# Kernel tuning notes

Hardware: AMD Instinct MI355X
Metric: run time of the kernel (lower is better)

The kernel has to match this reference:

```python
import jax, jax.numpy as jnp
import numpy as np

N = 50000      # nodes
E = 800000     # edges (avg degree 16)
F_IN = 256
F_OUT = 256


def setup_inputs() -> dict:
    key = jax.random.key(0)
    ks = jax.random.split(key, 8)
    feature = jax.random.normal(ks[0], (N, F_IN), dtype=jnp.float32)
    e_w = jax.random.uniform(ks[1], (E, 1), dtype=jnp.float32)
    snorm_n = jnp.ones((N, 1), dtype=jnp.float32)
    snorm_e = jnp.ones((E, 1), dtype=jnp.float32)
    src = jax.random.randint(ks[2], (E,), 0, N, dtype=jnp.int32)
    dst = jax.random.randint(ks[3], (E,), 0, N, dtype=jnp.int32)
    scale = 1.0 / np.sqrt(F_IN)
    W_self = jax.random.normal(ks[4], (F_IN, F_OUT), dtype=jnp.float32) * scale
    W = jax.random.normal(ks[5], (F_IN, F_OUT), dtype=jnp.float32) * scale
    b = jax.random.normal(ks[6], (F_OUT,), dtype=jnp.float32) * scale
    return {"feature": feature, "e_w": e_w, "snorm_n": snorm_n,
            "snorm_e": snorm_e, "W_self": W_self, "W": W, "b": b,
            "src": src, "dst": dst}


def reference(feature, e_w, snorm_n, snorm_e, W_self, W, b, src, dst):
    n = feature.shape[0]
    ones_e = jnp.ones_like(src, dtype=feature.dtype)
    # self transform
    h_s = feature @ W_self                                   # [N, F_OUT]
    # source-side degree normalization: deg_out^{-1/2}
    out_deg = jnp.maximum(jax.ops.segment_sum(ones_e, src, num_segments=n), 1.0)
    feat = feature * (out_deg ** -0.5)[:, None]              # [N, F_IN]
    # message = h[src] * e_w, aggregated by sum into dst (u_mul_e + sum reduce)
    msgs = feat[src] * e_w                                   # [E, F_IN]
    agg = jax.ops.segment_sum(msgs, dst, num_segments=n)     # [N, F_IN]
    # neighbor transform + destination-side degree normalization
    h = agg @ W + b                                          # [N, F_OUT]
    in_deg = jnp.maximum(jax.ops.segment_sum(ones_e, dst, num_segments=n), 1.0)
    h = h * (in_deg ** -0.5)[:, None]
    return h_s + h, e_w
```

## Files before the change

kernel.cpp:

```cpp
#include <hip/hip_runtime.h>
#include <hip/hip_bf16.h>

#define N_NODES 50000
#define N_EDGES 800000
#define MP      50048
#define MAXDEG  64

#define GEMM_BLOCKS  782
#define EDGE_BLOCKS  782
#define WCONV_BLOCKS 512

typedef __bf16 bf16x8_t __attribute__((ext_vector_type(8)));
typedef float  f32x4_t  __attribute__((ext_vector_type(4)));

__device__ __forceinline__ unsigned short f2bf(float x) {
  __hip_bfloat16 h = __float2bfloat16(x);
  return __builtin_bit_cast(unsigned short, h);
}
__device__ __forceinline__ float bf2f(unsigned short u) {
  unsigned int v = ((unsigned int)u) << 16;
  return __builtin_bit_cast(float, v);
}

__global__ __launch_bounds__(256) void wconv_kernel(
    const float* __restrict__ Wself, const float* __restrict__ W,
    unsigned short* __restrict__ Bt)
{
  int idx = blockIdx.x * 256 + threadIdx.x;
  int n = idx >> 8, k = idx & 255;
  float v = (n < 256) ? Wself[k * 256 + n] : W[k * 256 + (n - 256)];
  Bt[idx] = f2bf(v);
}

__global__ __launch_bounds__(256, 2) void gemm_edge_kernel(
    const float* __restrict__ feature,
    const unsigned short* __restrict__ Bt,
    const float* __restrict__ e_w, const int* __restrict__ src, const int* __restrict__ dst,
    int* __restrict__ cnt_in, int* __restrict__ cnt_out,
    unsigned int* __restrict__ bucket, float* __restrict__ out1,
    float* __restrict__ out0,
    unsigned char* __restrict__ y8)
{
  const int b   = blockIdx.x;
  const int tid = threadIdx.x;

  if (b & 1) {
    const int e0 = (b >> 1) * 1024 + tid;
#pragma unroll
    for (int k = 0; k < 4; ++k) {
      int e = e0 + k * 256;
      if (e < N_EDGES) {
        int s = src[e];
        int d = dst[e];
        float w = e_w[e];
        out1[e] = w;
        atomicAdd(&cnt_out[s], 1);
        int p = atomicAdd(&cnt_in[d], 1);
        if (p < MAXDEG) {
          unsigned int ent = ((unsigned int)f2bf(w) << 16) | (unsigned int)s;
          bucket[(size_t)d * MAXDEG + p] = ent;
        }
      }
    }
    return;
  }

  __shared__ __align__(16) unsigned short As[2][128 * 32];
  __shared__ __align__(16) unsigned short Bs[2][256 * 32];
  const int g    = b >> 1;
  const int half = g & 1;
  const int m0   = (g >> 1) * 128;
  const int n0   = half * 256;
  const int lane = tid & 63;
  const int wave = tid >> 6;
  const int wm = (wave & 1) * 64;
  const int wn = (wave >> 1) * 128;
  const int fr = lane & 15;
  const int fk = (lane >> 4) * 8;
  const int srow  = lane >> 2;
  const int scolb = (lane & 3) * 8;
  const bool full = (m0 + 128) <= N_NODES;

  f32x4_t acc[4][8] = {};

  for (int k0 = 0; k0 < 256; k0 += 64) {
#pragma unroll
    for (int p = 0; p < 2; ++p) {
      const int kk = k0 + p * 32;
#pragma unroll
      for (int j = 0; j < 4; ++j) {
        int rr = wave * 64 + j * 16;
        const unsigned short* gb = Bt + (size_t)(n0 + rr + srow) * 256 + (kk + scolb);
        __builtin_amdgcn_global_load_lds((const __attribute__((address_space(1))) void*)gb,
                                         (__attribute__((address_space(3))) void*)&Bs[p][rr * 32],
                                         16, 0, 0);
      }
#pragma unroll
      for (int j = 0; j < 2; ++j) {
        const int rr   = wave * 32 + j * 16 + srow;
        const int grow = m0 + rr;
        float4 v0 = {0.f, 0.f, 0.f, 0.f}, v1 = {0.f, 0.f, 0.f, 0.f};
        if (full || grow < N_NODES) {
          const float* ga = feature + (size_t)grow * 256 + (kk + scolb);
          v0 = *(const float4*)ga;
          v1 = *(const float4*)(ga + 4);
        }
        uint4 pk;
        pk.x = ((unsigned int)f2bf(v0.y) << 16) | (unsigned int)f2bf(v0.x);
        pk.y = ((unsigned int)f2bf(v0.w) << 16) | (unsigned int)f2bf(v0.z);
        pk.z = ((unsigned int)f2bf(v1.y) << 16) | (unsigned int)f2bf(v1.x);
        pk.w = ((unsigned int)f2bf(v1.w) << 16) | (unsigned int)f2bf(v1.z);
        *(uint4*)&As[p][rr * 32 + scolb] = pk;
      }
    }
    __syncthreads();

#pragma unroll
    for (int p = 0; p < 2; ++p) {
      bf16x8_t af[4], bfr[8];
#pragma unroll
      for (int i = 0; i < 4; ++i)
        af[i]  = *(const bf16x8_t*)&As[p][(wm + i * 16 + fr) * 32 + fk];
#pragma unroll
      for (int j = 0; j < 8; ++j)
        bfr[j] = *(const bf16x8_t*)&Bs[p][(wn + j * 16 + fr) * 32 + fk];
#pragma unroll
      for (int i = 0; i < 4; ++i)
#pragma unroll
        for (int j = 0; j < 8; ++j)
          acc[i][j] = __builtin_amdgcn_mfma_f32_16x16x32_bf16(af[i], bfr[j], acc[i][j], 0, 0, 0);
    }
    __syncthreads();
  }

  if (half == 0) {
#pragma unroll
    for (int i = 0; i < 4; ++i) {
      int rowb = m0 + wm + i * 16 + (lane >> 4) * 4;
#pragma unroll
      for (int j = 0; j < 8; ++j) {
        int col = wn + j * 16 + (lane & 15);
#pragma unroll
        for (int r = 0; r < 4; ++r) {
          int row = rowb + r;
          if (row < N_NODES)
            out0[(size_t)row * 256 + col] = acc[i][j][r];
        }
      }
    }
  } else {
#pragma unroll
    for (int i = 0; i < 4; ++i) {
      int rowb = m0 + wm + i * 16 + (lane >> 4) * 4;
#pragma unroll
      for (int j = 0; j < 8; ++j) {
        int col = wn + j * 16 + (lane & 15);
#pragma unroll
        for (int r = 0; r < 4; ++r) {
          int row = rowb + r;
          if (row < N_NODES) {
            float ys = acc[i][j][r];
            unsigned int pk = (unsigned int)__builtin_amdgcn_cvt_pk_fp8_f32(ys, ys, 0, false);
            y8[(size_t)row * 256 + col] = (unsigned char)(pk & 0xffu);
          }
        }
      }
    }
  }
}

__global__ __launch_bounds__(256) void agg_kernel(
    const unsigned char* __restrict__ y8, const unsigned int* __restrict__ bucket,
    const int* __restrict__ cnt_in, const int* __restrict__ cnt_out,
    const float* __restrict__ bias, float* __restrict__ out0)
{
  const int wave = threadIdx.x >> 6, lane = threadIdx.x & 63;
  const int node = blockIdx.x * 4 + wave;
  if (node >= N_NODES) return;
  int deg_raw = cnt_in[node];
  int deg = deg_raw > MAXDEG ? MAXDEG : deg_raw;

  unsigned int ent = 0u;
  if (lane < deg) ent = bucket[(size_t)node * MAXDEG + lane];
  int   sl = (int)(ent & 0xffffu);
  float wl = bf2f((unsigned short)(ent >> 16));
  int co = cnt_out[sl]; if (co < 1) co = 1;
  wl *= rsqrtf((float)co);

  float a0 = 0.f, a1 = 0.f, a2 = 0.f, a3 = 0.f;
  for (int bb = 0; bb < MAXDEG; bb += 16) {
    if (bb >= deg) break;
#pragma unroll
    for (int t = 0; t < 16; ++t) {
      int eb = bb + t;
      int   s = __shfl(sl, eb);
      float w = __shfl(wl, eb);
      bool ok = eb < deg;
      s = ok ? s : 0;
      w = ok ? w : 0.0f;
      unsigned int u = *(const unsigned int*)(y8 + (size_t)s * 256 + lane * 4);
      a0 += w * __builtin_amdgcn_cvt_f32_fp8(u, 0);
      a1 += w * __builtin_amdgcn_cvt_f32_fp8(u, 1);
      a2 += w * __builtin_amdgcn_cvt_f32_fp8(u, 2);
      a3 += w * __builtin_amdgcn_cvt_f32_fp8(u, 3);
    }
  }

  int dn = deg_raw < 1 ? 1 : deg_raw;
  float inv = rsqrtf((float)dn);
  float4 bc = *(const float4*)(bias + lane * 4);
  float4 o = *(float4*)(out0 + (size_t)node * 256 + lane * 4);
  o.x += (a0 + bc.x) * inv;
  o.y += (a1 + bc.y) * inv;
  o.z += (a2 + bc.z) * inv;
  o.w += (a3 + bc.w) * inv;
  *(float4*)(out0 + (size_t)node * 256 + lane * 4) = o;
}

extern "C" void kernel_launch(void* const* d_in, const int* in_sizes, int n_in,
                              void* d_out, int out_size, void* d_ws, size_t ws_size,
                              hipStream_t stream) {
  const float* feature = (const float*)d_in[0];
  const float* e_w     = (const float*)d_in[1];
  const float* W_self  = (const float*)d_in[4];
  const float* W       = (const float*)d_in[5];
  const float* bias    = (const float*)d_in[6];
  const int*   src     = (const int*)d_in[7];
  const int*   dst     = (const int*)d_in[8];

  float* out0 = (float*)d_out;
  float* out1 = out0 + (size_t)N_NODES * 256;

  char* ws = (char*)d_ws;
  int*            cnt_in  = (int*)(ws + 0);
  int*            cnt_out = (int*)(ws + 204800);
  unsigned int*   bucket  = (unsigned int*)(ws + 409600);
  unsigned short* Bt      = (unsigned short*)(ws + 13209600);
  unsigned char*  y8      = (unsigned char*)(ws + 13471744);

  hipMemsetAsync(ws, 0, 409600, stream);

  wconv_kernel<<<WCONV_BLOCKS, 256, 0, stream>>>(W_self, W, Bt);
  gemm_edge_kernel<<<GEMM_BLOCKS + EDGE_BLOCKS, 256, 0, stream>>>(
      feature, Bt, e_w, src, dst, cnt_in, cnt_out, bucket, out1, out0, y8);
  agg_kernel<<<(N_NODES + 3) / 4, 256, 0, stream>>>(y8, bucket, cnt_in, cnt_out, bias, out0);
}
```

Before: 260.5 us.

## Shrink GEMM tiles, software-pipeline loads with swizzled LDS, use half-wave aggregation

```diff
diff --git a/kernel.cpp b/kernel.cpp
--- a/kernel.cpp
+++ b/kernel.cpp
@@ -3,11 +3,12 @@
 
 #define N_NODES 50000
 #define N_EDGES 800000
-#define MP      50048
 #define MAXDEG  64
 
-#define GEMM_BLOCKS  782
+#define ROW_TILES    391
+#define GEMM_BLOCKS  1564
 #define EDGE_BLOCKS  782
+#define TOTAL_BLOCKS 2346
 #define WCONV_BLOCKS 512
 
 typedef __bf16 bf16x8_t __attribute__((ext_vector_type(8)));
@@ -20,6 +21,9 @@
 __device__ __forceinline__ float bf2f(unsigned short u) {
   unsigned int v = ((unsigned int)u) << 16;
   return __builtin_bit_cast(float, v);
+}
+__device__ __forceinline__ unsigned int pk2(float lo, float hi) {
+  return ((unsigned int)f2bf(hi) << 16) | (unsigned int)f2bf(lo);
 }
 
 __global__ __launch_bounds__(256) void wconv_kernel(
@@ -32,7 +36,7 @@
   Bt[idx] = f2bf(v);
 }
 
-__global__ __launch_bounds__(256, 2) void gemm_edge_kernel(
+__global__ __launch_bounds__(256, 4) void gemm_edge_kernel(
     const float* __restrict__ feature,
     const unsigned short* __restrict__ Bt,
     const float* __restrict__ e_w, const int* __restrict__ src, const int* __restrict__ dst,
@@ -44,8 +48,8 @@
   const int b   = blockIdx.x;
   const int tid = threadIdx.x;
 
-  if (b & 1) {
-    const int e0 = (b >> 1) * 1024 + tid;
+  if (b % 3 == 2) {
+    const int e0 = (b / 3) * 1024 + tid;
 #pragma unroll
     for (int k = 0; k < 4; ++k) {
       int e = e0 + k * 256;
@@ -66,80 +70,112 @@
   }
 
   __shared__ __align__(16) unsigned short As[2][128 * 32];
-  __shared__ __align__(16) unsigned short Bs[2][256 * 32];
-  const int g    = b >> 1;
-  const int half = g & 1;
-  const int m0   = (g >> 1) * 128;
-  const int n0   = half * 256;
+  __shared__ __align__(16) unsigned short Bs[2][128 * 32];
+
+  const int g    = (b / 3) * 2 + (b % 3);
+  const int q    = g & 3;
+  const int m0   = (g >> 2) * 128;
+  const int bn0  = q * 128;
   const int lane = tid & 63;
   const int wave = tid >> 6;
-  const int wm = (wave & 1) * 64;
-  const int wn = (wave >> 1) * 128;
-  const int fr = lane & 15;
-  const int fk = (lane >> 4) * 8;
-  const int srow  = lane >> 2;
-  const int scolb = (lane & 3) * 8;
-  const bool full = (m0 + 128) <= N_NODES;
-
-  f32x4_t acc[4][8] = {};
-
-  for (int k0 = 0; k0 < 256; k0 += 64) {
-#pragma unroll
-    for (int p = 0; p < 2; ++p) {
-      const int kk = k0 + p * 32;
-#pragma unroll
-      for (int j = 0; j < 4; ++j) {
-        int rr = wave * 64 + j * 16;
-        const unsigned short* gb = Bt + (size_t)(n0 + rr + srow) * 256 + (kk + scolb);
+  const int wm   = (wave & 1) * 64;
+  const int wn   = (wave >> 1) * 64;
+  const int fr   = lane & 15;
+  const int fkc  = lane >> 4;
+
+  const int ra = tid >> 1, ha = tid & 1;
+  const int sA = (ra >> 1) & 3;
+  const int arow = (m0 + ra < N_NODES) ? (m0 + ra) : 0;
+  const float* aptr = feature + (size_t)arow * 256;
+  const int cg0 = (2 * ha) ^ sA;
+  const int cg1 = (2 * ha + 1) ^ sA;
+  const int aw0 = ra * 32 + (2 * ha) * 8;
+  const int aw1 = aw0 + 8;
+
+  f32x4_t acc[4][4] = {};
+
+  {
+#pragma unroll
+    for (int i = 0; i < 2; ++i) {
+      int r  = i * 64 + (tid >> 2);
+      int cg = (tid & 3) ^ ((r >> 1) & 3);
+      const unsigned short* gb = Bt + (size_t)(bn0 + r) * 256 + cg * 8;
+      __builtin_amdgcn_global_load_lds((const __attribute__((address_space(1))) void*)gb,
+                                       (__attribute__((address_space(3))) void*)&Bs[0][i * 2048 + wave * 512],
+                                       16, 0, 0);
+    }
+    float4 a0 = *(const float4*)(aptr + cg0 * 8);
+    float4 a1 = *(const float4*)(aptr + cg0 * 8 + 4);
+    float4 a2 = *(const float4*)(aptr + cg1 * 8);
+    float4 a3 = *(const float4*)(aptr + cg1 * 8 + 4);
+    uint4 p0, p1;
+    p0.x = pk2(a0.x, a0.y); p0.y = pk2(a0.z, a0.w);
+    p0.z = pk2(a1.x, a1.y); p0.w = pk2(a1.z, a1.w);
+    p1.x = pk2(a2.x, a2.y); p1.y = pk2(a2.z, a2.w);
+    p1.z = pk2(a3.x, a3.y); p1.w = pk2(a3.z, a3.w);
+    *(uint4*)&As[0][aw0] = p0;
+    *(uint4*)&As[0][aw1] = p1;
+  }
+  __syncthreads();
+
+#pragma unroll
+  for (int s = 0; s < 8; ++s) {
+    const int cb = s & 1, nb = cb ^ 1;
+    float4 a0, a1, a2, a3;
+    if (s < 7) {
+      const int k0 = (s + 1) * 32;
+#pragma unroll
+      for (int i = 0; i < 2; ++i) {
+        int r  = i * 64 + (tid >> 2);
+        int cg = (tid & 3) ^ ((r >> 1) & 3);
+        const unsigned short* gb = Bt + (size_t)(bn0 + r) * 256 + k0 + cg * 8;
         __builtin_amdgcn_global_load_lds((const __attribute__((address_space(1))) void*)gb,
-                                         (__attribute__((address_space(3))) void*)&Bs[p][rr * 32],
+                                         (__attribute__((address_space(3))) void*)&Bs[nb][i * 2048 + wave * 512],
                                          16, 0, 0);
       }
-#pragma unroll
-      for (int j = 0; j < 2; ++j) {
-        const int rr   = wave * 32 + j * 16 + srow;
-        const int grow = m0 + rr;
-        float4 v0 = {0.f, 0.f, 0.f, 0.f}, v1 = {0.f, 0.f, 0.f, 0.f};
-        if (full || grow < N_NODES) {
-          const float* ga = feature + (size_t)grow * 256 + (kk + scolb);
-          v0 = *(const float4*)ga;
-          v1 = *(const float4*)(ga + 4);
-        }
-        uint4 pk;
-        pk.x = ((unsigned int)f2bf(v0.y) << 16) | (unsigned int)f2bf(v0.x);
-        pk.y = ((unsigned int)f2bf(v0.w) << 16) | (unsigned int)f2bf(v0.z);
-        pk.z = ((unsigned int)f2bf(v1.y) << 16) | (unsigned int)f2bf(v1.x);
-        pk.w = ((unsigned int)f2bf(v1.w) << 16) | (unsigned int)f2bf(v1.z);
-        *(uint4*)&As[p][rr * 32 + scolb] = pk;
-      }
-    }
-    __syncthreads();
-
-#pragma unroll
-    for (int p = 0; p < 2; ++p) {
-      bf16x8_t af[4], bfr[8];
-#pragma unroll
-      for (int i = 0; i < 4; ++i)
-        af[i]  = *(const bf16x8_t*)&As[p][(wm + i * 16 + fr) * 32 + fk];
-#pragma unroll
-      for (int j = 0; j < 8; ++j)
-        bfr[j] = *(const bf16x8_t*)&Bs[p][(wn + j * 16 + fr) * 32 + fk];
-#pragma unroll
-      for (int i = 0; i < 4; ++i)
-#pragma unroll
-        for (int j = 0; j < 8; ++j)
-          acc[i][j] = __builtin_amdgcn_mfma_f32_16x16x32_bf16(af[i], bfr[j], acc[i][j], 0, 0, 0);
-    }
-    __syncthreads();
-  }
-
-  if (half == 0) {
+      a0 = *(const float4*)(aptr + k0 + cg0 * 8);
+      a1 = *(const float4*)(aptr + k0 + cg0 * 8 + 4);
+      a2 = *(const float4*)(aptr + k0 + cg1 * 8);
+      a3 = *(const float4*)(aptr + k0 + cg1 * 8 + 4);
+    }
+
+    bf16x8_t af[4], bv[4];
+#pragma unroll
+    for (int i = 0; i < 4; ++i) {
+      int R = wm + i * 16 + fr;
+      af[i] = *(const bf16x8_t*)&As[cb][R * 32 + ((fkc ^ ((R >> 1) & 3)) * 8)];
+    }
+#pragma unroll
+    for (int j = 0; j < 4; ++j) {
+      int R = wn + j * 16 + fr;
+      bv[j] = *(const bf16x8_t*)&Bs[cb][R * 32 + ((fkc ^ ((R >> 1) & 3)) * 8)];
+    }
+#pragma unroll
+    for (int i = 0; i < 4; ++i)
+#pragma unroll
+      for (int j = 0; j < 4; ++j)
+        acc[i][j] = __builtin_amdgcn_mfma_f32_16x16x32_bf16(af[i], bv[j], acc[i][j], 0, 0, 0);
+
+    if (s < 7) {
+      uint4 p0, p1;
+      p0.x = pk2(a0.x, a0.y); p0.y = pk2(a0.z, a0.w);
+      p0.z = pk2(a1.x, a1.y); p0.w = pk2(a1.z, a1.w);
+      p1.x = pk2(a2.x, a2.y); p1.y = pk2(a2.z, a2.w);
+      p1.z = pk2(a3.x, a3.y); p1.w = pk2(a3.z, a3.w);
+      *(uint4*)&As[nb][aw0] = p0;
+      *(uint4*)&As[nb][aw1] = p1;
+      __syncthreads();
+    }
+  }
+
+  if (q < 2) {
+    const int cbase = q * 128 + wn + (lane & 15);
 #pragma unroll
     for (int i = 0; i < 4; ++i) {
       int rowb = m0 + wm + i * 16 + (lane >> 4) * 4;
 #pragma unroll
-      for (int j = 0; j < 8; ++j) {
-        int col = wn + j * 16 + (lane & 15);
+      for (int j = 0; j < 4; ++j) {
+        int col = cbase + j * 16;
 #pragma unroll
         for (int r = 0; r < 4; ++r) {
           int row = rowb + r;
@@ -149,12 +185,13 @@
       }
     }
   } else {
+    const int cbase = (q - 2) * 128 + wn + (lane & 15);
 #pragma unroll
     for (int i = 0; i < 4; ++i) {
       int rowb = m0 + wm + i * 16 + (lane >> 4) * 4;
 #pragma unroll
-      for (int j = 0; j < 8; ++j) {
-        int col = wn + j * 16 + (lane & 15);
+      for (int j = 0; j < 4; ++j) {
+        int col = cbase + j * 16;
 #pragma unroll
         for (int r = 0; r < 4; ++r) {
           int row = rowb + r;
@@ -174,47 +211,59 @@
     const int* __restrict__ cnt_in, const int* __restrict__ cnt_out,
     const float* __restrict__ bias, float* __restrict__ out0)
 {
-  const int wave = threadIdx.x >> 6, lane = threadIdx.x & 63;
-  const int node = blockIdx.x * 4 + wave;
+  const int hw   = threadIdx.x >> 5;
+  const int lane = threadIdx.x & 31;
+  const int node = blockIdx.x * 8 + hw;
   if (node >= N_NODES) return;
   int deg_raw = cnt_in[node];
   int deg = deg_raw > MAXDEG ? MAXDEG : deg_raw;
 
-  unsigned int ent = 0u;
-  if (lane < deg) ent = bucket[(size_t)node * MAXDEG + lane];
-  int   sl = (int)(ent & 0xffffu);
-  float wl = bf2f((unsigned short)(ent >> 16));
-  int co = cnt_out[sl]; if (co < 1) co = 1;
-  wl *= rsqrtf((float)co);
-
   float a0 = 0.f, a1 = 0.f, a2 = 0.f, a3 = 0.f;
-  for (int bb = 0; bb < MAXDEG; bb += 16) {
+  float a4 = 0.f, a5 = 0.f, a6 = 0.f, a7 = 0.f;
+
+  for (int bb = 0; bb < MAXDEG; bb += 32) {
     if (bb >= deg) break;
-#pragma unroll
-    for (int t = 0; t < 16; ++t) {
-      int eb = bb + t;
-      int   s = __shfl(sl, eb);
-      float w = __shfl(wl, eb);
-      bool ok = eb < deg;
-      s = ok ? s : 0;
-      w = ok ? w : 0.0f;
-      unsigned int u = *(const unsigned int*)(y8 + (size_t)s * 256 + lane * 4);
-      a0 += w * __builtin_amdgcn_cvt_f32_fp8(u, 0);
-      a1 += w * __builtin_amdgcn_cvt_f32_fp8(u, 1);
-      a2 += w * __builtin_amdgcn_cvt_f32_fp8(u, 2);
-      a3 += w * __builtin_amdgcn_cvt_f32_fp8(u, 3);
+    int idx = bb + lane;
+    unsigned int ent = (idx < deg) ? bucket[(size_t)node * MAXDEG + idx] : 0u;
+    int   sl = (int)(ent & 0xffffu);
+    float wl = bf2f((unsigned short)(ent >> 16));
+    int co = cnt_out[sl]; if (co < 1) co = 1;
+    wl *= rsqrtf((float)co);
+
+#pragma unroll
+    for (int t0 = 0; t0 < 32; t0 += 16) {
+      if (bb + t0 >= deg) break;
+#pragma unroll
+      for (int t = 0; t < 16; ++t) {
+        int eb = t0 + t;
+        int   s = __shfl(sl, eb, 32);
+        float w = __shfl(wl, eb, 32);
+        uint2 u = *(const uint2*)(y8 + (size_t)s * 256 + lane * 8);
+        a0 += w * __builtin_amdgcn_cvt_f32_fp8(u.x, 0);
+        a1 += w * __builtin_amdgcn_cvt_f32_fp8(u.x, 1);
+        a2 += w * __builtin_amdgcn_cvt_f32_fp8(u.x, 2);
+        a3 += w * __builtin_amdgcn_cvt_f32_fp8(u.x, 3);
+        a4 += w * __builtin_amdgcn_cvt_f32_fp8(u.y, 0);
+        a5 += w * __builtin_amdgcn_cvt_f32_fp8(u.y, 1);
+        a6 += w * __builtin_amdgcn_cvt_f32_fp8(u.y, 2);
+        a7 += w * __builtin_amdgcn_cvt_f32_fp8(u.y, 3);
+      }
     }
   }
 
   int dn = deg_raw < 1 ? 1 : deg_raw;
   float inv = rsqrtf((float)dn);
-  float4 bc = *(const float4*)(bias + lane * 4);
-  float4 o = *(float4*)(out0 + (size_t)node * 256 + lane * 4);
-  o.x += (a0 + bc.x) * inv;
-  o.y += (a1 + bc.y) * inv;
-  o.z += (a2 + bc.z) * inv;
-  o.w += (a3 + bc.w) * inv;
-  *(float4*)(out0 + (size_t)node * 256 + lane * 4) = o;
+  float4 b0 = *(const float4*)(bias + lane * 8);
+  float4 b1 = *(const float4*)(bias + lane * 8 + 4);
+  size_t off = (size_t)node * 256 + lane * 8;
+  float4 o0 = *(float4*)(out0 + off);
+  float4 o1 = *(float4*)(out0 + off + 4);
+  o0.x += (a0 + b0.x) * inv;  o0.y += (a1 + b0.y) * inv;
+  o0.z += (a2 + b0.z) * inv;  o0.w += (a3 + b0.w) * inv;
+  o1.x += (a4 + b1.x) * inv;  o1.y += (a5 + b1.y) * inv;
+  o1.z += (a6 + b1.z) * inv;  o1.w += (a7 + b1.w) * inv;
+  *(float4*)(out0 + off)     = o0;
+  *(float4*)(out0 + off + 4) = o1;
 }
 
 extern "C" void kernel_launch(void* const* d_in, const int* in_sizes, int n_in,
@@ -241,7 +290,7 @@
   hipMemsetAsync(ws, 0, 409600, stream);
 
   wconv_kernel<<<WCONV_BLOCKS, 256, 0, stream>>>(W_self, W, Bt);
-  gemm_edge_kernel<<<GEMM_BLOCKS + EDGE_BLOCKS, 256, 0, stream>>>(
+  gemm_edge_kernel<<<TOTAL_BLOCKS, 256, 0, stream>>>(
       feature, Bt, e_w, src, dst, cnt_in, cnt_out, bucket, out1, out0, y8);
-  agg_kernel<<<(N_NODES + 3) / 4, 256, 0, stream>>>(y8, bucket, cnt_in, cnt_out, bias, out0);
-}
+  agg_kernel<<<(N_NODES + 7) / 8, 256, 0, stream>>>(y8, bucket, cnt_in, cnt_out, bias, out0);
+}
```

Measured after the change: 256.1 us. Within noise of the previous version (-1.7%).
